# Kernel tuning notes

Measured on AMD Instinct MI355X. Metric: run time of the kernel, lower is better.

Reference implementation:

```python
import jax, jax.numpy as jnp
import numpy as np

B, Z, NOBS = 16384, 64, 2
D = Z + NOBS  # update_mlp_in_size
H1, H2 = 16, 16
HC1, HC2 = 32, 32


def setup_inputs() -> dict:
    key = jax.random.key(0)
    ks = jax.random.split(key, 20)
    inp = {}
    inp['latents'] = jax.random.normal(ks[0], (B, Z), jnp.float32)
    inp['obs'] = jax.random.normal(ks[1], (B, NOBS), jnp.float32)
    # reparameterization noise (torch.randn_like equivalents, made explicit)
    inp['noise_update'] = jax.random.normal(ks[2], (B, D, Z), jnp.float32)
    inp['noise_global'] = jax.random.normal(ks[3], (B, Z), jnp.float32)
    # parameters
    inp['z_0'] = jax.random.normal(ks[4], (Z,), jnp.float32)
    inp['mult_u'] = jnp.ones((D, Z), jnp.float32)
    inp['logvar_u'] = jax.random.uniform(ks[5], (D, Z), jnp.float32, -3.0, -2.0)
    inp['mult_g'] = jnp.ones((Z,), jnp.float32)
    inp['logvar_g'] = jax.random.uniform(ks[6], (Z,), jnp.float32, -3.0, -2.0)
    # per-latent update MLPs, batched over Z
    s = lambda fan_in: 1.0 / np.sqrt(fan_in)
    inp['W1'] = jax.random.uniform(ks[7], (Z, D, H1), jnp.float32, -s(D), s(D))
    inp['b1'] = jax.random.uniform(ks[8], (Z, H1), jnp.float32, -s(D), s(D))
    inp['W2'] = jax.random.uniform(ks[9], (Z, H1, H2), jnp.float32, -s(H1), s(H1))
    inp['b2'] = jax.random.uniform(ks[10], (Z, H2), jnp.float32, -s(H1), s(H1))
    inp['W3'] = jax.random.uniform(ks[11], (Z, H2, 2), jnp.float32, -s(H2), s(H2))
    inp['b3'] = jax.random.uniform(ks[12], (Z, 2), jnp.float32, -s(H2), s(H2))
    # choice MLP (include_stimulus=False -> input dim Z)
    inp['Wc1'] = jax.random.uniform(ks[13], (Z, HC1), jnp.float32, -s(Z), s(Z))
    inp['bc1'] = jax.random.uniform(ks[14], (HC1,), jnp.float32, -s(Z), s(Z))
    inp['Wc2'] = jax.random.uniform(ks[15], (HC1, HC2), jnp.float32, -s(HC1), s(HC1))
    inp['bc2'] = jax.random.uniform(ks[16], (HC2,), jnp.float32, -s(HC1), s(HC1))
    inp['Wc3'] = jax.random.uniform(ks[17], (HC2, 2), jnp.float32, -s(HC2), s(HC2))
    inp['bc3'] = jax.random.uniform(ks[18], (2,), jnp.float32, -s(HC2), s(HC2))
    inp['t_0'] = 0  # False
    return inp


def reference(latents, obs, noise_update, noise_global, z_0, mult_u, logvar_u,
              mult_g, logvar_g, W1, b1, W2, b2, W3, b3,
              Wc1, bc1, Wc2, bc2, Wc3, bc3, t_0):
    lat = jnp.broadcast_to(z_0, latents.shape) if t_0 else latents  # [B,Z]
    x = jnp.concatenate([lat, obs], axis=-1)  # [B,D]
    # --- per-latent update bottlenecks, vectorized over Z ---
    var_u = jnp.exp(logvar_u)                      # [D,Z]
    mean_u = x[:, :, None] * mult_u[None]          # [B,D,Z]
    kld_u = -0.5 * jnp.sum(1.0 + logvar_u[None] - mean_u ** 2 - var_u[None], axis=1)  # [B,Z]
    x_tilde = noise_update * jnp.sqrt(var_u)[None] + mean_u  # [B,D,Z]
    # --- per-latent tiny MLPs, batched as grouped GEMMs ---
    h = jax.nn.relu(jnp.einsum('bdz,zdh->bzh', x_tilde, W1) + b1[None])
    h = jax.nn.relu(jnp.einsum('bzh,zhk->bzk', h, W2) + b2[None])
    o = jnp.einsum('bzk,zko->bzo', h, W3) + b3[None]          # [B,Z,2]
    u = o[..., 0]
    w = jax.nn.sigmoid(o[..., 1])
    new_latents = (1.0 - w) * lat + u * w          # gated update, [B,Z]
    # --- global bottleneck ---
    var_g = jnp.exp(logvar_g)
    mean_g = mult_g * new_latents
    kld_g = -0.5 * jnp.sum(1.0 + logvar_g - mean_g ** 2 - var_g, axis=-1)  # [B]
    z_tilde = noise_global * jnp.sqrt(var_g) + mean_g
    # --- choice MLP (no stimulus) ---
    y = jax.nn.relu(z_tilde @ Wc1 + bc1)
    y = jax.nn.relu(y @ Wc2 + bc2)
    y = y @ Wc3 + bc3                              # [B,2]
    return (y, z_tilde, kld_g, kld_u)
```

## Files before the change

### kernel.cpp

```cpp
#include <hip/hip_runtime.h>
#include <hip/hip_bf16.h>
#include <stdint.h>

#define BB 16384
#define ZZ 64
#define DD 66
#define NB 4
#define WPB 4

#define OFF_SVMU 0
#define OFF_C0U  8448
#define OFF_MG   8512
#define OFF_SVG  8576
#define OFF_C0G  8640

__global__ void prep_kernel(const float* __restrict__ mult_u, const float* __restrict__ logvar_u,
                            const float* __restrict__ mult_g, const float* __restrict__ logvar_g,
                            float* __restrict__ ws) {
  const int t = threadIdx.x;
  for (int i = t; i < DD*ZZ; i += 256) {
    ws[OFF_SVMU + 2*i]     = mult_u[i];
    ws[OFF_SVMU + 2*i + 1] = __expf(0.5f * logvar_u[i]);
  }
  if (t < ZZ) {
    float s = 0.f;
    for (int d = 0; d < DD; ++d) {
      const float lv = logvar_u[d*ZZ + t];
      s += 1.f + lv - __expf(lv);
    }
    ws[OFF_C0U + t] = -0.5f * s;
    ws[OFF_MG  + t] = mult_g[t];
    ws[OFF_SVG + t] = __expf(0.5f * logvar_g[t]);
  }
  if (t == 0) {
    float s = 0.f;
    for (int z = 0; z < ZZ; ++z) {
      const float lv = logvar_g[z];
      s += 1.f + lv - __expf(lv);
    }
    ws[OFF_C0G] = -0.5f * s;
  }
}

__global__ __launch_bounds__(256, 2)
void disrnn_main(const float* __restrict__ latents, const float* __restrict__ obs,
                 const float* __restrict__ noise_u, const float* __restrict__ noise_g,
                 const float* __restrict__ z0, const float* __restrict__ W1,
                 const float* __restrict__ b1, const float* __restrict__ W2,
                 const float* __restrict__ b2, const float* __restrict__ W3,
                 const float* __restrict__ b3,
                 const float* __restrict__ ws, const int* __restrict__ t0p,
                 float* __restrict__ out) {
  float* out_zt = out + BB*2;
  float* out_kg = out + BB*2 + BB*ZZ;
  float* out_ku = out + BB*2 + BB*ZZ + BB;

  __shared__ float x_lds[WPB][NB][68];
  __shared__ float red[WPB][NB][64];

  const int tid  = threadIdx.x;
  const int w    = tid >> 6;
  const int lane = tid & 63;
  const int b0   = (blockIdx.x * WPB + w) * NB;
  const int t0   = *t0p;

  const float c0u_l = ws[OFF_C0U + lane];
  const float mg_l  = ws[OFF_MG + lane];
  const float svg_l = ws[OFF_SVG + lane];
  const float c0g   = ws[OFF_C0G];
  const float b3_0  = b3[lane*2];
  const float b3_1  = b3[lane*2 + 1];
  const float2* __restrict__ svmu = (const float2*)(ws + OFF_SVMU);

#pragma unroll
  for (int i = 0; i < NB; ++i) {
    x_lds[w][i][lane] = t0 ? z0[lane] : latents[(b0 + i)*ZZ + lane];
    if (lane < 2) x_lds[w][i][ZZ + lane] = obs[(b0 + i)*2 + lane];
  }
  __syncthreads();

  float acc[NB][16], kacc[NB];
  {
    const float4* bp = reinterpret_cast<const float4*>(b1 + lane*16);
    float b1r[16];
#pragma unroll
    for (int q = 0; q < 4; ++q) {
      const float4 v = bp[q];
      b1r[4*q] = v.x; b1r[4*q+1] = v.y; b1r[4*q+2] = v.z; b1r[4*q+3] = v.w;
    }
#pragma unroll
    for (int i = 0; i < NB; ++i) {
      kacc[i] = 0.f;
#pragma unroll
      for (int h = 0; h < 16; ++h) acc[i][h] = b1r[h];
    }
  }

  for (int d = 0; d < DD; ++d) {
    const float2 sm = svmu[d*ZZ + lane];
    const float4* wp = reinterpret_cast<const float4*>(W1 + (lane*DD + d)*16);
    float wv[16];
#pragma unroll
    for (int q = 0; q < 4; ++q) {
      const float4 v = wp[q];
      wv[4*q] = v.x; wv[4*q+1] = v.y; wv[4*q+2] = v.z; wv[4*q+3] = v.w;
    }
#pragma unroll
    for (int i = 0; i < NB; ++i) {
      const float xv   = x_lds[w][i][d];
      const float mean = xv * sm.x;
      const float nv   = noise_u[((b0 + i)*DD + d)*ZZ + lane];
      const float xt   = fmaf(nv, sm.y, mean);
      kacc[i] = fmaf(mean, mean, kacc[i]);
#pragma unroll
      for (int h = 0; h < 16; ++h) acc[i][h] = fmaf(xt, wv[h], acc[i][h]);
    }
  }

  float h2[NB][16];
  {
    const float4* bp = reinterpret_cast<const float4*>(b2 + lane*16);
    float b2r[16];
#pragma unroll
    for (int q = 0; q < 4; ++q) {
      const float4 v = bp[q];
      b2r[4*q] = v.x; b2r[4*q+1] = v.y; b2r[4*q+2] = v.z; b2r[4*q+3] = v.w;
    }
#pragma unroll
    for (int i = 0; i < NB; ++i) {
#pragma unroll
      for (int h = 0; h < 16; ++h) acc[i][h] = fmaxf(acc[i][h], 0.f);
#pragma unroll
      for (int k = 0; k < 16; ++k) h2[i][k] = b2r[k];
    }
  }
  for (int h = 0; h < 16; ++h) {
    const float4* wp = reinterpret_cast<const float4*>(W2 + (lane*16 + h)*16);
    float wv[16];
#pragma unroll
    for (int q = 0; q < 4; ++q) {
      const float4 v = wp[q];
      wv[4*q] = v.x; wv[4*q+1] = v.y; wv[4*q+2] = v.z; wv[4*q+3] = v.w;
    }
#pragma unroll
    for (int i = 0; i < NB; ++i) {
      const float hv = acc[i][h];
#pragma unroll
      for (int k = 0; k < 16; ++k) h2[i][k] = fmaf(hv, wv[k], h2[i][k]);
    }
  }

  float w3r[32];
  {
    const float4* wp = reinterpret_cast<const float4*>(W3 + lane*32);
#pragma unroll
    for (int q = 0; q < 8; ++q) {
      const float4 v = wp[q];
      w3r[4*q] = v.x; w3r[4*q+1] = v.y; w3r[4*q+2] = v.z; w3r[4*q+3] = v.w;
    }
  }
#pragma unroll
  for (int i = 0; i < NB; ++i) {
    const int b = b0 + i;
    float o0 = b3_0, o1 = b3_1;
#pragma unroll
    for (int k = 0; k < 16; ++k) {
      const float hv = fmaxf(h2[i][k], 0.f);
      o0 = fmaf(hv, w3r[2*k], o0);
      o1 = fmaf(hv, w3r[2*k + 1], o1);
    }
    const float xl = x_lds[w][i][lane];
    const float wg = 1.f / (1.f + __expf(-o1));
    const float nl = fmaf(wg, o0 - xl, xl);
    const float tg = mg_l * nl;
    const float zt = fmaf(noise_g[b*ZZ + lane], svg_l, tg);
    out_zt[b*ZZ + lane] = zt;
    out_ku[b*ZZ + lane] = fmaf(0.5f, kacc[i], c0u_l);
    red[w][i][lane] = tg * tg;
  }
  __syncthreads();
  if (lane < NB) {
    float s = 0.f;
    for (int z = 0; z < ZZ; ++z) s += red[w][lane][z];
    out_kg[b0 + lane] = fmaf(0.5f, s, c0g);
  }
}

__global__ __launch_bounds__(256, 2)
void choice_kernel(const float* __restrict__ Wc1, const float* __restrict__ bc1,
                   const float* __restrict__ Wc2, const float* __restrict__ bc2,
                   const float* __restrict__ Wc3, const float* __restrict__ bc3,
                   float* __restrict__ out) {
  const float* zt_in = out + BB*2;
  float* out_y = out;

  __shared__ float zl[WPB][64];
  __shared__ float y1[WPB][32];
  __shared__ float y2[WPB][32];

  const int tid  = threadIdx.x;
  const int w    = tid >> 6;
  const int lane = tid & 63;
  const int b    = blockIdx.x * WPB + w;

  zl[w][lane] = zt_in[b*ZZ + lane];
  __syncthreads();
  if (lane < 32) {
    float a = bc1[lane];
    for (int z = 0; z < 64; ++z) a = fmaf(zl[w][z], Wc1[z*32 + lane], a);
    y1[w][lane] = fmaxf(a, 0.f);
  }
  __syncthreads();
  if (lane < 32) {
    float a = bc2[lane];
    for (int h = 0; h < 32; ++h) a = fmaf(y1[w][h], Wc2[h*32 + lane], a);
    y2[w][lane] = fmaxf(a, 0.f);
  }
  __syncthreads();
  if (lane == 0) {
    float s0 = bc3[0], s1 = bc3[1];
    for (int k = 0; k < 32; ++k) {
      s0 = fmaf(y2[w][k], Wc3[2*k], s0);
      s1 = fmaf(y2[w][k], Wc3[2*k + 1], s1);
    }
    out_y[b*2]     = s0;
    out_y[b*2 + 1] = s1;
  }
}

extern "C" void kernel_launch(void* const* d_in, const int* in_sizes, int n_in,
                              void* d_out, int out_size, void* d_ws, size_t ws_size,
                              hipStream_t stream) {
  const float* latents  = (const float*)d_in[0];
  const float* obs      = (const float*)d_in[1];
  const float* noise_u  = (const float*)d_in[2];
  const float* noise_g  = (const float*)d_in[3];
  const float* z0       = (const float*)d_in[4];
  const float* mult_u   = (const float*)d_in[5];
  const float* logvar_u = (const float*)d_in[6];
  const float* mult_g   = (const float*)d_in[7];
  const float* logvar_g = (const float*)d_in[8];
  const float* W1       = (const float*)d_in[9];
  const float* b1       = (const float*)d_in[10];
  const float* W2       = (const float*)d_in[11];
  const float* b2       = (const float*)d_in[12];
  const float* W3       = (const float*)d_in[13];
  const float* b3       = (const float*)d_in[14];
  const float* Wc1      = (const float*)d_in[15];
  const float* bc1      = (const float*)d_in[16];
  const float* Wc2      = (const float*)d_in[17];
  const float* bc2      = (const float*)d_in[18];
  const float* Wc3      = (const float*)d_in[19];
  const float* bc3      = (const float*)d_in[20];
  const int*  t0p       = (const int*)d_in[21];
  float* ws = (float*)d_ws;
  float* outp = (float*)d_out;

  prep_kernel<<<1, 256, 0, stream>>>(mult_u, logvar_u, mult_g, logvar_g, ws);
  disrnn_main<<<BB/(WPB*NB), 256, 0, stream>>>(latents, obs, noise_u, noise_g, z0,
                                               W1, b1, W2, b2, W3, b3,
                                               ws, t0p, outp);
  choice_kernel<<<BB/WPB, 256, 0, stream>>>(Wc1, bc1, Wc2, bc2, Wc3, bc3, outp);
}
```

Measured before the change: 614.7 us.

## Transpose MLP weights for coalesced loads, fuse choice MLP, prefetch noise

The prep kernel now runs across 66 blocks and also writes W1, W2 and W3 into a transposed layout. With that layout, each lane's float4 weight loads are interleaved across lanes and coalesce, where before each lane read a strided per-latent row. The main loop software-pipelines the noise, weight and x loads one to two steps ahead. Rows per wave drop from 4 to 2 with launch bounds raised to 4 blocks per CU for occupancy. The global KL reduction now uses wave shuffles, and the choice MLP is fused into the main kernel, removing the third launch and the re-read of z_tilde.

New measurement: 732.9 us. 19.2% more time.

```diff
diff --git a/kernel.cpp b/kernel.cpp
--- a/kernel.cpp
+++ b/kernel.cpp
@@ -1,54 +1,78 @@
 #include <hip/hip_runtime.h>
-#include <hip/hip_bf16.h>
 #include <stdint.h>
 
 #define BB 16384
 #define ZZ 64
 #define DD 66
-#define NB 4
+#define NB 2
 #define WPB 4
+#define ROWS (WPB*NB)
 
 #define OFF_SVMU 0
 #define OFF_C0U  8448
 #define OFF_MG   8512
 #define OFF_SVG  8576
 #define OFF_C0G  8640
+#define OFF_W1T  8704
+#define OFF_W2T  76288
+#define OFF_W3T  92672
 
 __global__ void prep_kernel(const float* __restrict__ mult_u, const float* __restrict__ logvar_u,
                             const float* __restrict__ mult_g, const float* __restrict__ logvar_g,
-                            float* __restrict__ ws) {
+                            const float* __restrict__ W1, const float* __restrict__ W2,
+                            const float* __restrict__ W3, float* __restrict__ ws) {
+  const int d = blockIdx.x;
   const int t = threadIdx.x;
-  for (int i = t; i < DD*ZZ; i += 256) {
-    ws[OFF_SVMU + 2*i]     = mult_u[i];
-    ws[OFF_SVMU + 2*i + 1] = __expf(0.5f * logvar_u[i]);
+  const int z = t >> 2, q = t & 3;
+
+  {
+    const float4 v = *reinterpret_cast<const float4*>(W1 + (z*DD + d)*16 + q*4);
+    *reinterpret_cast<float4*>(ws + OFF_W1T + ((d*4 + q)*64 + z)*4) = v;
   }
   if (t < ZZ) {
-    float s = 0.f;
-    for (int d = 0; d < DD; ++d) {
-      const float lv = logvar_u[d*ZZ + t];
-      s += 1.f + lv - __expf(lv);
-    }
-    ws[OFF_C0U + t] = -0.5f * s;
-    ws[OFF_MG  + t] = mult_g[t];
-    ws[OFF_SVG + t] = __expf(0.5f * logvar_g[t]);
-  }
-  if (t == 0) {
-    float s = 0.f;
-    for (int z = 0; z < ZZ; ++z) {
-      const float lv = logvar_g[z];
-      s += 1.f + lv - __expf(lv);
-    }
-    ws[OFF_C0G] = -0.5f * s;
+    ws[OFF_SVMU + 2*(d*ZZ + t)]     = mult_u[d*ZZ + t];
+    ws[OFF_SVMU + 2*(d*ZZ + t) + 1] = __expf(0.5f * logvar_u[d*ZZ + t]);
+  }
+  if (d < 16) {
+    const float4 v = *reinterpret_cast<const float4*>(W2 + (z*16 + d)*16 + q*4);
+    *reinterpret_cast<float4*>(ws + OFF_W2T + ((d*4 + q)*64 + z)*4) = v;
+  }
+  if (d == 16 || d == 17) {
+    const int idx = (d - 16)*256 + t;
+    const int qq = idx >> 6, zz = idx & 63;
+    const float4 v = *reinterpret_cast<const float4*>(W3 + zz*32 + qq*4);
+    *reinterpret_cast<float4*>(ws + OFF_W3T + (qq*64 + zz)*4) = v;
+  }
+  if (d == 0) {
+    if (t < ZZ) {
+      float s = 0.f;
+      for (int dd = 0; dd < DD; ++dd) {
+        const float lv = logvar_u[dd*ZZ + t];
+        s += 1.f + lv - __expf(lv);
+      }
+      ws[OFF_C0U + t] = -0.5f * s;
+      ws[OFF_MG  + t] = mult_g[t];
+      ws[OFF_SVG + t] = __expf(0.5f * logvar_g[t]);
+    }
+    if (t == 0) {
+      float s = 0.f;
+      for (int zc = 0; zc < ZZ; ++zc) {
+        const float lv = logvar_g[zc];
+        s += 1.f + lv - __expf(lv);
+      }
+      ws[OFF_C0G] = -0.5f * s;
+    }
   }
 }
 
-__global__ __launch_bounds__(256, 2)
+__global__ __launch_bounds__(256, 4)
 void disrnn_main(const float* __restrict__ latents, const float* __restrict__ obs,
                  const float* __restrict__ noise_u, const float* __restrict__ noise_g,
-                 const float* __restrict__ z0, const float* __restrict__ W1,
-                 const float* __restrict__ b1, const float* __restrict__ W2,
-                 const float* __restrict__ b2, const float* __restrict__ W3,
-                 const float* __restrict__ b3,
+                 const float* __restrict__ z0, const float* __restrict__ b1,
+                 const float* __restrict__ b2, const float* __restrict__ b3,
+                 const float* __restrict__ Wc1, const float* __restrict__ bc1,
+                 const float* __restrict__ Wc2, const float* __restrict__ bc2,
+                 const float* __restrict__ Wc3, const float* __restrict__ bc3,
                  const float* __restrict__ ws, const int* __restrict__ t0p,
                  float* __restrict__ out) {
   float* out_zt = out + BB*2;
@@ -56,7 +80,9 @@
   float* out_ku = out + BB*2 + BB*ZZ + BB;
 
   __shared__ float x_lds[WPB][NB][68];
-  __shared__ float red[WPB][NB][64];
+  __shared__ float ztl[ROWS][64];
+  __shared__ float y1[ROWS][32];
+  __shared__ float y2[ROWS][32];
 
   const int tid  = threadIdx.x;
   const int w    = tid >> 6;
@@ -64,20 +90,17 @@
   const int b0   = (blockIdx.x * WPB + w) * NB;
   const int t0   = *t0p;
 
+#pragma unroll
+  for (int i = 0; i < NB; ++i) {
+    x_lds[w][i][lane] = t0 ? z0[lane] : latents[(b0 + i)*ZZ + lane];
+    if (lane < 2) x_lds[w][i][ZZ + lane] = obs[(b0 + i)*2 + lane];
+  }
+  __syncthreads();
+
   const float c0u_l = ws[OFF_C0U + lane];
   const float mg_l  = ws[OFF_MG + lane];
   const float svg_l = ws[OFF_SVG + lane];
   const float c0g   = ws[OFF_C0G];
-  const float b3_0  = b3[lane*2];
-  const float b3_1  = b3[lane*2 + 1];
-  const float2* __restrict__ svmu = (const float2*)(ws + OFF_SVMU);
-
-#pragma unroll
-  for (int i = 0; i < NB; ++i) {
-    x_lds[w][i][lane] = t0 ? z0[lane] : latents[(b0 + i)*ZZ + lane];
-    if (lane < 2) x_lds[w][i][ZZ + lane] = obs[(b0 + i)*2 + lane];
-  }
-  __syncthreads();
 
   float acc[NB][16], kacc[NB];
   {
@@ -96,25 +119,57 @@
     }
   }
 
+  const float*  w1t  = ws + OFF_W1T;
+  const float2* svmu = reinterpret_cast<const float2*>(ws + OFF_SVMU);
+  const float* np[NB];
+#pragma unroll
+  for (int i = 0; i < NB; ++i) np[i] = noise_u + (b0 + i)*DD*ZZ + lane;
+
+  float nv_c[NB], nv_n[NB];
+#pragma unroll
+  for (int i = 0; i < NB; ++i) { nv_c[i] = np[i][0]; nv_n[i] = np[i][ZZ]; }
+  float wv_c[16];
+#pragma unroll
+  for (int q = 0; q < 4; ++q) {
+    const float4 v = *reinterpret_cast<const float4*>(w1t + (q*64 + lane)*4);
+    wv_c[4*q] = v.x; wv_c[4*q+1] = v.y; wv_c[4*q+2] = v.z; wv_c[4*q+3] = v.w;
+  }
+  float2 sm_c = svmu[lane];
+  float xv_c[NB];
+#pragma unroll
+  for (int i = 0; i < NB; ++i) xv_c[i] = x_lds[w][i][0];
+
+#pragma unroll 2
   for (int d = 0; d < DD; ++d) {
-    const float2 sm = svmu[d*ZZ + lane];
-    const float4* wp = reinterpret_cast<const float4*>(W1 + (lane*DD + d)*16);
-    float wv[16];
+    const int dn  = (d + 1 < DD) ? d + 1 : DD - 1;
+    const int dnn = (d + 2 < DD) ? d + 2 : DD - 1;
+    float nv2[NB];
+#pragma unroll
+    for (int i = 0; i < NB; ++i) nv2[i] = np[i][dnn*ZZ];
+    float wv_n[16];
 #pragma unroll
     for (int q = 0; q < 4; ++q) {
-      const float4 v = wp[q];
-      wv[4*q] = v.x; wv[4*q+1] = v.y; wv[4*q+2] = v.z; wv[4*q+3] = v.w;
-    }
+      const float4 v = *reinterpret_cast<const float4*>(w1t + ((dn*4 + q)*64 + lane)*4);
+      wv_n[4*q] = v.x; wv_n[4*q+1] = v.y; wv_n[4*q+2] = v.z; wv_n[4*q+3] = v.w;
+    }
+    const float2 sm_n = svmu[dn*ZZ + lane];
+    float xv_n[NB];
+#pragma unroll
+    for (int i = 0; i < NB; ++i) xv_n[i] = x_lds[w][i][dn];
+
 #pragma unroll
     for (int i = 0; i < NB; ++i) {
-      const float xv   = x_lds[w][i][d];
-      const float mean = xv * sm.x;
-      const float nv   = noise_u[((b0 + i)*DD + d)*ZZ + lane];
-      const float xt   = fmaf(nv, sm.y, mean);
+      const float mean = xv_c[i] * sm_c.x;
       kacc[i] = fmaf(mean, mean, kacc[i]);
-#pragma unroll
-      for (int h = 0; h < 16; ++h) acc[i][h] = fmaf(xt, wv[h], acc[i][h]);
-    }
+      const float xt = fmaf(nv_c[i], sm_c.y, mean);
+#pragma unroll
+      for (int h = 0; h < 16; ++h) acc[i][h] = fmaf(xt, wv_c[h], acc[i][h]);
+    }
+#pragma unroll
+    for (int i = 0; i < NB; ++i) { nv_c[i] = nv_n[i]; nv_n[i] = nv2[i]; xv_c[i] = xv_n[i]; }
+#pragma unroll
+    for (int h = 0; h < 16; ++h) wv_c[h] = wv_n[h];
+    sm_c = sm_n;
   }
 
   float h2[NB][16];
@@ -134,35 +189,37 @@
       for (int k = 0; k < 16; ++k) h2[i][k] = b2r[k];
     }
   }
+  const float* w2t = ws + OFF_W2T;
+#pragma unroll
   for (int h = 0; h < 16; ++h) {
-    const float4* wp = reinterpret_cast<const float4*>(W2 + (lane*16 + h)*16);
-    float wv[16];
+    float wv2[16];
 #pragma unroll
     for (int q = 0; q < 4; ++q) {
-      const float4 v = wp[q];
-      wv[4*q] = v.x; wv[4*q+1] = v.y; wv[4*q+2] = v.z; wv[4*q+3] = v.w;
+      const float4 v = *reinterpret_cast<const float4*>(w2t + ((h*4 + q)*64 + lane)*4);
+      wv2[4*q] = v.x; wv2[4*q+1] = v.y; wv2[4*q+2] = v.z; wv2[4*q+3] = v.w;
     }
 #pragma unroll
     for (int i = 0; i < NB; ++i) {
       const float hv = acc[i][h];
 #pragma unroll
-      for (int k = 0; k < 16; ++k) h2[i][k] = fmaf(hv, wv[k], h2[i][k]);
+      for (int k = 0; k < 16; ++k) h2[i][k] = fmaf(hv, wv2[k], h2[i][k]);
     }
   }
 
   float w3r[32];
   {
-    const float4* wp = reinterpret_cast<const float4*>(W3 + lane*32);
+    const float* w3t = ws + OFF_W3T;
 #pragma unroll
     for (int q = 0; q < 8; ++q) {
-      const float4 v = wp[q];
+      const float4 v = *reinterpret_cast<const float4*>(w3t + (q*64 + lane)*4);
       w3r[4*q] = v.x; w3r[4*q+1] = v.y; w3r[4*q+2] = v.z; w3r[4*q+3] = v.w;
     }
   }
+  const float2 b3v = reinterpret_cast<const float2*>(b3)[lane];
 #pragma unroll
   for (int i = 0; i < NB; ++i) {
     const int b = b0 + i;
-    float o0 = b3_0, o1 = b3_1;
+    float o0 = b3v.x, o1 = b3v.y;
 #pragma unroll
     for (int k = 0; k < 16; ++k) {
       const float hv = fmaxf(h2[i][k], 0.f);
@@ -176,61 +233,43 @@
     const float zt = fmaf(noise_g[b*ZZ + lane], svg_l, tg);
     out_zt[b*ZZ + lane] = zt;
     out_ku[b*ZZ + lane] = fmaf(0.5f, kacc[i], c0u_l);
-    red[w][i][lane] = tg * tg;
+    ztl[w*NB + i][lane] = zt;
+    float t2 = tg * tg;
+#pragma unroll
+    for (int off = 32; off; off >>= 1) t2 += __shfl_xor(t2, off);
+    if (lane == 0) out_kg[b] = fmaf(0.5f, t2, c0g);
   }
   __syncthreads();
-  if (lane < NB) {
-    float s = 0.f;
-    for (int z = 0; z < ZZ; ++z) s += red[w][lane][z];
-    out_kg[b0 + lane] = fmaf(0.5f, s, c0g);
-  }
-}
-
-__global__ __launch_bounds__(256, 2)
-void choice_kernel(const float* __restrict__ Wc1, const float* __restrict__ bc1,
-                   const float* __restrict__ Wc2, const float* __restrict__ bc2,
-                   const float* __restrict__ Wc3, const float* __restrict__ bc3,
-                   float* __restrict__ out) {
-  const float* zt_in = out + BB*2;
-  float* out_y = out;
-
-  __shared__ float zl[WPB][64];
-  __shared__ float y1[WPB][32];
-  __shared__ float y2[WPB][32];
-
-  const int tid  = threadIdx.x;
-  const int w    = tid >> 6;
-  const int lane = tid & 63;
-  const int b    = blockIdx.x * WPB + w;
-
-  zl[w][lane] = zt_in[b*ZZ + lane];
+
+  const int r  = tid >> 5;
+  const int hc = tid & 31;
+  {
+    float a = bc1[hc];
+#pragma unroll
+    for (int zc = 0; zc < 64; ++zc) a = fmaf(ztl[r][zc], Wc1[zc*32 + hc], a);
+    y1[r][hc] = fmaxf(a, 0.f);
+  }
   __syncthreads();
-  if (lane < 32) {
-    float a = bc1[lane];
-    for (int z = 0; z < 64; ++z) a = fmaf(zl[w][z], Wc1[z*32 + lane], a);
-    y1[w][lane] = fmaxf(a, 0.f);
+  {
+    float a = bc2[hc];
+#pragma unroll
+    for (int k = 0; k < 32; ++k) a = fmaf(y1[r][k], Wc2[k*32 + hc], a);
+    y2[r][hc] = fmaxf(a, 0.f);
   }
   __syncthreads();
-  if (lane < 32) {
-    float a = bc2[lane];
-    for (int h = 0; h < 32; ++h) a = fmaf(y1[w][h], Wc2[h*32 + lane], a);
-    y2[w][lane] = fmaxf(a, 0.f);
-  }
-  __syncthreads();
-  if (lane == 0) {
-    float s0 = bc3[0], s1 = bc3[1];
-    for (int k = 0; k < 32; ++k) {
-      s0 = fmaf(y2[w][k], Wc3[2*k], s0);
-      s1 = fmaf(y2[w][k], Wc3[2*k + 1], s1);
-    }
-    out_y[b*2]     = s0;
-    out_y[b*2 + 1] = s1;
+  if (tid < ROWS*2) {
+    const int rr = tid >> 1, o = tid & 1;
+    float s = bc3[o];
+#pragma unroll
+    for (int k = 0; k < 32; ++k) s = fmaf(y2[rr][k], Wc3[2*k + o], s);
+    out[(blockIdx.x*ROWS + rr)*2 + o] = s;
   }
 }
 
 extern "C" void kernel_launch(void* const* d_in, const int* in_sizes, int n_in,
                               void* d_out, int out_size, void* d_ws, size_t ws_size,
                               hipStream_t stream) {
+  (void)in_sizes; (void)n_in; (void)out_size; (void)ws_size;
   const float* latents  = (const float*)d_in[0];
   const float* obs      = (const float*)d_in[1];
   const float* noise_u  = (const float*)d_in[2];
@@ -253,12 +292,11 @@
   const float* Wc3      = (const float*)d_in[19];
   const float* bc3      = (const float*)d_in[20];
   const int*  t0p       = (const int*)d_in[21];
-  float* ws = (float*)d_ws;
+  float* ws   = (float*)d_ws;
   float* outp = (float*)d_out;
 
-  prep_kernel<<<1, 256, 0, stream>>>(mult_u, logvar_u, mult_g, logvar_g, ws);
-  disrnn_main<<<BB/(WPB*NB), 256, 0, stream>>>(latents, obs, noise_u, noise_g, z0,
-                                               W1, b1, W2, b2, W3, b3,
-                                               ws, t0p, outp);
-  choice_kernel<<<BB/WPB, 256, 0, stream>>>(Wc1, bc1, Wc2, bc2, Wc3, bc3, outp);
+  prep_kernel<<<66, 256, 0, stream>>>(mult_u, logvar_u, mult_g, logvar_g, W1, W2, W3, ws);
+  disrnn_main<<<BB/ROWS, 256, 0, stream>>>(latents, obs, noise_u, noise_g, z0,
+                                           b1, b2, b3, Wc1, bc1, Wc2, bc2, Wc3, bc3,
+                                           ws, t0p, outp);
 }
```
